# Performance work log

Measured on AMD Instinct MI355X. Metric: run time of the kernel, lower is better.

Reference implementation:

```python
import jax, jax.numpy as jnp
import numpy as np

# ---- fixed configuration (from init_kwargs / sensor='WV3', ratio=4) ----
B, NBANDS, H, W = 4, 8, 512, 512
RATIO = 4
BETA = 0.25
KSIZE = 41                    # MTF kernel size used by gen_mtf
SCALE = 2                     # ceil(ratio / 2), StructuralLoss half-window
MASK_HW = 8                   # half-window used by local_corr_mask
MTF_R = MTF_C = 2             # strided scatter offsets in SpectralLossNocorr
EPS = 1e-20
# WV3 Nyquist gains (one per MS band)
GNYQ = np.asarray([0.325, 0.355, 0.360, 0.350, 0.365, 0.360, 0.335, 0.315])


def gen_mtf_kernel():
    """Per-band Gaussian MTF filter, shape (NBANDS, 1, K, K), sum-normalized."""
    fcut = 1.0 / RATIO
    ax = np.arange(KSIZE) - (KSIZE - 1) / 2.0
    xx, yy = np.meshgrid(ax, ax)
    kerns = []
    for g in GNYQ:
        alpha = np.sqrt(((KSIZE - 1) * (fcut / 2.0)) ** 2 / (-2.0 * np.log(g)))
        k = np.exp(-(xx ** 2 + yy ** 2) / (2.0 * alpha ** 2))
        kerns.append(k / k.sum())
    return np.stack(kerns, axis=0)[:, None].astype(np.float32)


def _boxsum(x, w):
    """Sum over a 2w x 2w sliding window via double cumsum (matches torch ref)."""
    x = jnp.pad(x, ((0, 0), (0, 0), (w, w), (w, w)))
    c = jnp.cumsum(jnp.cumsum(x, axis=-1), axis=-2)
    return (c[..., 2 * w:, 2 * w:] - c[..., :-2 * w, 2 * w:]
            - c[..., 2 * w:, :-2 * w] + c[..., :-2 * w, :-2 * w])


def _xcorr(a, b, w):
    """Local cross-correlation (xcorr_torch). a:(B,Ca,H,W), b:(B,Cb,H,W) broadcast."""
    n = 4.0 * w * w
    da = a - _boxsum(a, w) / n
    db = b - _boxsum(b, w) / n
    s_ab = _boxsum(da * db, w)
    s_aa = _boxsum(da * da, w)
    s_bb = _boxsum(db * db, w)
    return s_ab / (jnp.sqrt(s_aa * s_bb) + EPS)


def _depthconv(x, kern):
    # torch Conv2d(groups=nbands, padding='same') == grouped cross-correlation
    return jax.lax.conv_general_dilated(
        x, kern, (1, 1), 'SAME', feature_group_count=kern.shape[0],
        dimension_numbers=('NCHW', 'OIHW', 'NCHW'))


def _local_corr_mask(inp, kern):
    pan = inp[:, -1:, :, :]          # (B,1,H,W)
    ms = inp[:, :-1, :, :]           # (B,NB,H,W)
    k0 = kern[0:1]                   # first-band MTF kernel (1,1,K,K)
    pad = (KSIZE - 1) // 2
    pan = jnp.pad(pan, ((0, 0), (0, 0), (pad, pad), (pad, pad)), mode='edge')
    pan = jax.lax.conv_general_dilated(
        pan, k0, (1, 1), 'VALID', dimension_numbers=('NCHW', 'OIHW', 'NCHW'))
    return 1.0 - _xcorr(pan, ms, MASK_HW)  # (B,NB,H,W)


def setup_inputs() -> dict:
    key = jax.random.key(0)
    k1, k2, k3 = jax.random.split(key, 3)
    return {
        'outputs': jax.random.normal(k1, (B, NBANDS, H, W), jnp.float32),
        'labels': jax.random.uniform(k2, (B, NBANDS + 1, H, W), jnp.float32),
        'inp': jax.random.uniform(k3, (B, NBANDS + 1, H, W), jnp.float32),
        'mtf_kernel': jnp.asarray(gen_mtf_kernel()),           # frozen param
        'spec_mask': jnp.ones((1, NBANDS, H, W), jnp.float32),  # buffer
    }


def reference(outputs, labels, inp, mtf_kernel, spec_mask):
    # ---- SpectralLossNocorr ----
    x = _depthconv(outputs, mtf_kernel)                      # (B,NB,H,W)
    labels_spec = labels[:, :-1]
    sub = labels_spec[:, :, 2::RATIO, 2::RATIO]              # (B,NB,H/4,W/4)
    y = jnp.zeros_like(x).at[:, :, MTF_R::RATIO, MTF_C::RATIO].set(sub)
    msub = jnp.broadcast_to(spec_mask[:, :, 2::RATIO, 2::RATIO], sub.shape)
    Wm = jnp.zeros_like(x).at[:, :, MTF_R::RATIO, MTF_C::RATIO].set(msub)
    Wm = Wm / jnp.sum(Wm)
    L_spec = jnp.sum(jnp.abs(x * Wm - y * Wm))
    # ---- StructuralLoss (with local_corr_mask threshold) ----
    pan = labels[:, -1:, :, :]
    thr = _local_corr_mask(inp, mtf_kernel)                  # (B,NB,H,W)
    Xc = jnp.maximum(_xcorr(outputs, pan, SCALE), -1.0)      # clamp(min=-1)
    X = 1.0 - Xc
    Y = X * (X > thr)                                        # keep worst pixels
    L_struct = jnp.mean(Y)
    return L_spec + BETA * L_struct
```

## Files before the change

kernel.cpp:

```cpp
#include <hip/hip_runtime.h>
#include <hip/hip_bf16.h>

#define HWSZ   262144
#define IMG    512
#define NBATCH 4
#define NBANDS 8

typedef _Float16 half_t;
typedef _Float16 half2v __attribute__((ext_vector_type(2)));
typedef _Float16 half4v __attribute__((ext_vector_type(4)));
typedef _Float16 half8v __attribute__((ext_vector_type(8)));

__device__ __forceinline__ void blockReduceAtomicAdd(double v, double* target,
                                                     double* red) {
    for (int off = 32; off > 0; off >>= 1) v += __shfl_down(v, off, 64);
    const int wave = threadIdx.x >> 6, lane = threadIdx.x & 63;
    if (lane == 0) red[wave] = v;
    __syncthreads();
    if (threadIdx.x == 0) atomicAdd(target, red[0] + red[1] + red[2] + red[3]);
}

__global__ __launch_bounds__(256) void k_pan_h(const float* __restrict__ inp,
                                               const float* __restrict__ mtf,
                                               float* __restrict__ tmpH) {
    __shared__ float seg[296];
    __shared__ float vrow[41];
    const int tid = threadIdx.x;
    const int b = blockIdx.z, r = blockIdx.y, c0 = blockIdx.x * 256;
    if (tid < 41) vrow[tid] = mtf[20 * 41 + tid] / sqrtf(mtf[20 * 41 + 20]);
    const float* pan = inp + ((long)b * 9 + 8) * HWSZ + (long)r * IMG;
    for (int e = tid; e < 296; e += 256) {
        int c = c0 - 20 + e;
        c = min(max(c, 0), IMG - 1);
        seg[e] = pan[c];
    }
    __syncthreads();
    float s = 0.f;
#pragma unroll
    for (int j = 0; j < 41; ++j) s += vrow[j] * seg[tid + j];
    tmpH[(long)b * HWSZ + (long)r * IMG + c0 + tid] = s;
}

__global__ __launch_bounds__(256) void k_pan_v(const float* __restrict__ tmpH,
                                               const float* __restrict__ mtf,
                                               float* __restrict__ panf) {
    __shared__ float ucol[41];
    const int tid = threadIdx.x;
    const int b = blockIdx.z, r = blockIdx.y, c = blockIdx.x * 256 + tid;
    if (tid < 41) ucol[tid] = mtf[tid * 41 + 20] / sqrtf(mtf[20 * 41 + 20]);
    __syncthreads();
    const float* base = tmpH + (long)b * HWSZ;
    float s = 0.f;
#pragma unroll
    for (int i = 0; i < 41; ++i) {
        int rr = min(max(r - 20 + i, 0), IMG - 1);
        s += ucol[i] * base[(long)rr * IMG + c];
    }
    panf[(long)b * HWSZ + (long)r * IMG + c] = s;
}

template <int W>
__global__ __launch_bounds__(256) void k_da(const float* __restrict__ in,
                                            long inBatchStride,
                                            float* __restrict__ out) {
    constexpr int TS = 32, WIN = 2 * W, NN = 4 * W * W, RE = TS + WIN - 1;
    constexpr int SR = RE;
    constexpr int ST = 33;
    __shared__ float RAW[RE * SR];
    __shared__ float T[RE * ST];
    const int tid = threadIdx.x;
    const int tr0 = blockIdx.y * TS, tc0 = blockIdx.x * TS;
    const float* src = in + (long)blockIdx.z * inBatchStride;
    for (int e = tid; e < RE * RE; e += 256) {
        int r = e / RE, c = e % RE;
        int gr = tr0 - (W - 1) + r, gc = tc0 - (W - 1) + c;
        float v = 0.f;
        if (gr >= 0 && gr < IMG && gc >= 0 && gc < IMG) v = src[(long)gr * IMG + gc];
        RAW[r * SR + c] = v;
    }
    __syncthreads();
    for (int e = tid; e < RE * TS; e += 256) {
        int r = e >> 5, j = e & 31;
        float s = 0.f;
#pragma unroll
        for (int k = 0; k < WIN; ++k) s += RAW[r * SR + j + k];
        T[r * ST + j] = s;
    }
    __syncthreads();
    float* dst = out + (long)blockIdx.z * HWSZ;
    for (int e = tid; e < TS * TS; e += 256) {
        int pr = e >> 5, pc = e & 31;
        float s = 0.f;
#pragma unroll
        for (int k = 0; k < WIN; ++k) s += T[(pr + k) * ST + pc];
        float da = RAW[(pr + W - 1) * SR + (pc + W - 1)] - s * (1.0f / NN);
        dst[(long)(tr0 + pr) * IMG + tc0 + pc] = da;
    }
}

template <int W>
__global__ __launch_bounds__(256) void k_sq(const float* __restrict__ in,
                                            float* __restrict__ out) {
    constexpr int TS = 32, WIN = 2 * W, RE = TS + WIN - 1;
    constexpr int SR = RE, ST = 33;
    __shared__ float RAW[RE * SR];
    __shared__ float T[RE * ST];
    const int tid = threadIdx.x;
    const int tr0 = blockIdx.y * TS, tc0 = blockIdx.x * TS;
    const float* src = in + (long)blockIdx.z * HWSZ;
    for (int e = tid; e < RE * RE; e += 256) {
        int r = e / RE, c = e % RE;
        int gr = tr0 - (W - 1) + r, gc = tc0 - (W - 1) + c;
        float v = 0.f;
        if (gr >= 0 && gr < IMG && gc >= 0 && gc < IMG) v = src[(long)gr * IMG + gc];
        RAW[r * SR + c] = v;
    }
    __syncthreads();
    for (int e = tid; e < RE * TS; e += 256) {
        int r = e >> 5, j = e & 31;
        float s = 0.f;
#pragma unroll
        for (int k = 0; k < WIN; ++k) {
            float v = RAW[r * SR + j + k];
            s += v * v;
        }
        T[r * ST + j] = s;
    }
    __syncthreads();
    float* dst = out + (long)blockIdx.z * HWSZ;
    for (int e = tid; e < TS * TS; e += 256) {
        int pr = e >> 5, pc = e & 31;
        float s = 0.f;
#pragma unroll
        for (int k = 0; k < WIN; ++k) s += T[(pr + k) * ST + pc];
        dst[(long)(tr0 + pr) * IMG + tc0 + pc] = s;
    }
}


template <int W> struct WinDims {
    static constexpr int A  = (W + 3) & ~3;
    static constexpr int NU = A + W + 8;
    static constexpr int NF = (NU + 3) / 4;
    static constexpr int NV = NF * 4;
};

template <int W>
__device__ __forceinline__ void loadRowWin(const float* __restrict__ row, int c0,
                                           float* v) {
    constexpr int A = WinDims<W>::A;
    constexpr int NF = WinDims<W>::NF;
#pragma unroll
    for (int f = 0; f < NF; ++f) {
        const int cb = c0 - A + 4 * f;
        if (cb >= 0 && cb + 3 < IMG) {
            const float4 t = *(const float4*)(row + cb);
            v[4 * f + 0] = t.x; v[4 * f + 1] = t.y;
            v[4 * f + 2] = t.z; v[4 * f + 3] = t.w;
        } else {
#pragma unroll
            for (int u = 0; u < 4; ++u) {
                const int c = cb + u;
                v[4 * f + u] = (c >= 0 && c < IMG) ? row[c] : 0.f;
            }
        }
    }
}

template <int W>
__device__ __forceinline__ void loadRowWinH(const half_t* __restrict__ row, int c0,
                                            float* v) {
    constexpr int A = WinDims<W>::A;
    constexpr int NF = WinDims<W>::NF;
#pragma unroll
    for (int f = 0; f < NF; ++f) {
        const int cb = c0 - A + 4 * f;
        if (cb >= 0 && cb + 3 < IMG) {
            const half4v t = *(const half4v*)(row + cb);
            v[4 * f + 0] = (float)t[0]; v[4 * f + 1] = (float)t[1];
            v[4 * f + 2] = (float)t[2]; v[4 * f + 3] = (float)t[3];
        } else {
#pragma unroll
            for (int u = 0; u < 4; ++u) {
                const int c = cb + u;
                v[4 * f + u] = (c >= 0 && c < IMG) ? (float)row[c] : 0.f;
            }
        }
    }
}

template <int W>
__global__ __launch_bounds__(256) void kHbox(const float* __restrict__ in,
                                             long sB, long sC,
                                             half_t* __restrict__ out) {
    constexpr int A = WinDims<W>::A;
    const int g = blockIdx.x * 256 + threadIdx.x;
    const int c0 = (g & 63) << 3, r = (g >> 6) & 511, z = g >> 15;
    const float* row = in + (long)(z >> 3) * sB + (long)(z & 7) * sC + (long)r * IMG;
    float v[WinDims<W>::NV];
    loadRowWin<W>(row, c0, v);
    float o[8];
    float s = 0.f;
#pragma unroll
    for (int i = A - W + 1; i <= A + W; ++i) s += v[i];
    o[0] = s;
#pragma unroll
    for (int j = 1; j < 8; ++j) {
        s += v[A + W + j] - v[A - W + j];
        o[j] = s;
    }
    half8v h;
#pragma unroll
    for (int j = 0; j < 8; ++j) h[j] = (half_t)o[j];
    *(half8v*)(out + (long)z * HWSZ + (long)r * IMG + c0) = h;
}

template <int W>
__global__ __launch_bounds__(256) void kVda(const half_t* __restrict__ t,
                                            const float* __restrict__ orig,
                                            long sB, long sC,
                                            half_t* __restrict__ out) {
    constexpr int NR = 2 * W + 15, NN = 4 * W * W;
    const int g = blockIdx.x * 256 + threadIdx.x;
    const int cp = (g & 255) * 2;
    const int rc = (g >> 8) & 31, z = g >> 13;
    const int r0 = rc * 16;
    const half_t* tz = t + (long)z * HWSZ + cp;
    float vx[NR], vy[NR];
#pragma unroll
    for (int i = 0; i < NR; ++i) {
        const int rr = r0 - W + 1 + i;
        if (rr >= 0 && rr < IMG) {
            const half2v h = *(const half2v*)(tz + (long)rr * IMG);
            vx[i] = (float)h[0]; vy[i] = (float)h[1];
        } else { vx[i] = 0.f; vy[i] = 0.f; }
    }
    const float* oz = orig + (long)(z >> 3) * sB + (long)(z & 7) * sC + cp;
    half_t* dst = out + (long)z * HWSZ + cp;
    float sx = 0.f, sy = 0.f;
#pragma unroll
    for (int i = 0; i < 2 * W; ++i) { sx += vx[i]; sy += vy[i]; }
#pragma unroll
    for (int j = 0; j < 16; ++j) {
        const float2 o = *(const float2*)(oz + (long)(r0 + j) * IMG);
        half2v h;
        h[0] = (half_t)(o.x - sx * (1.0f / NN));
        h[1] = (half_t)(o.y - sy * (1.0f / NN));
        *(half2v*)(dst + (long)(r0 + j) * IMG) = h;
        if (j < 15) {
            sx += vx[2 * W + j] - vx[j];
            sy += vy[2 * W + j] - vy[j];
        }
    }
}


template <int W>
__device__ __forceinline__ void stageProducts(const half_t* __restrict__ daz,
                                              const float* __restrict__ dsz,
                                              int tr0, int tc0,
                                              unsigned int* L) {
    constexpr int A = WinDims<W>::A;
    constexpr int NU = WinDims<W>::NU;
    constexpr int NV = WinDims<W>::NV;
    constexpr int NRS = 63 + 2 * W;
    constexpr int LP = 65;
    for (int e = threadIdx.x; e < NRS * 8; e += 256) {
        const int i = e >> 3, cg = e & 7;
        const int gr = tr0 - W + 1 + i;
        const int c0 = tc0 + cg * 8;
        unsigned int* dst = L + i * LP + cg * 8;
        if (gr < 0 || gr >= IMG) {
#pragma unroll
            for (int j = 0; j < 8; ++j) dst[j] = 0u;
            continue;
        }
        float va[NV], vs[NV];
        loadRowWinH<W>(daz + (long)gr * IMG, c0, va);
        loadRowWin<W>(dsz + (long)gr * IMG, c0, vs);
        float p1[NV], p2[NV];
#pragma unroll
        for (int k = 0; k < NU; ++k) { p1[k] = va[k] * vs[k]; p2[k] = va[k] * va[k]; }
        float s1 = 0.f, s2 = 0.f;
#pragma unroll
        for (int k = A - W + 1; k <= A + W; ++k) { s1 += p1[k]; s2 += p2[k]; }
#pragma unroll
        for (int j = 0; j < 8; ++j) {
            half2v h;
            h[0] = (half_t)s1; h[1] = (half_t)s2;
            dst[j] = __builtin_bit_cast(unsigned int, h);
            if (j < 7) {
                s1 += p1[A + W + 1 + j] - p1[A - W + 1 + j];
                s2 += p2[A + W + 1 + j] - p2[A - W + 1 + j];
            }
        }
    }
}

__global__ __launch_bounds__(256) void kFusedThr(const half_t* __restrict__ daMS,
                                                 const float* __restrict__ daPAN,
                                                 const float* __restrict__ saa,
                                                 half_t* __restrict__ thr) {
    constexpr int W = 8, LP = 65, NRS = 63 + 2 * W;
    __shared__ unsigned int L[NRS * LP];
    const int z = blockIdx.z, b = z >> 3;
    const int tr0 = blockIdx.y * 64, tc0 = blockIdx.x * 64;
    stageProducts<W>(daMS + (long)z * HWSZ, daPAN + (long)b * HWSZ, tr0, tc0, L);
    __syncthreads();
    const int c = threadIdx.x & 63, q = threadIdx.x >> 6;
    const int ro0 = q * 16;
    float s1 = 0.f, s2 = 0.f;
#pragma unroll
    for (int k = 0; k < 2 * W; ++k) {
        const half2v h = __builtin_bit_cast(half2v, L[(ro0 + k) * LP + c]);
        s1 += (float)h[0]; s2 += (float)h[1];
    }
    const float* sz = saa + (long)b * HWSZ + tc0 + c;
    half_t* tz = thr + (long)z * HWSZ + tc0 + c;
#pragma unroll
    for (int j = 0; j < 16; ++j) {
        const int r = tr0 + ro0 + j;
        const float sa = sz[(long)r * IMG];
        const float den = sqrtf(fmaxf(sa * s2, 0.f)) + 1e-20f;
        tz[(long)r * IMG] = (half_t)(1.0f - s1 / den);
        if (j < 15) {
            const half2v ha = __builtin_bit_cast(half2v, L[(ro0 + j + 2 * W) * LP + c]);
            const half2v hs = __builtin_bit_cast(half2v, L[(ro0 + j) * LP + c]);
            s1 += (float)ha[0] - (float)hs[0];
            s2 += (float)ha[1] - (float)hs[1];
        }
    }
}

__global__ __launch_bounds__(256) void kFusedY(const half_t* __restrict__ daOUT,
                                               const float* __restrict__ dbPAN,
                                               const float* __restrict__ sbb,
                                               const half_t* __restrict__ thr,
                                               double* __restrict__ acc) {
    constexpr int W = 2, LP = 65, NRS = 63 + 2 * W;
    __shared__ unsigned int L[NRS * LP];
    __shared__ double red[4];
    const int z = blockIdx.z, b = z >> 3;
    const int tr0 = blockIdx.y * 64, tc0 = blockIdx.x * 64;
    stageProducts<W>(daOUT + (long)z * HWSZ, dbPAN + (long)b * HWSZ, tr0, tc0, L);
    __syncthreads();
    const int c = threadIdx.x & 63, q = threadIdx.x >> 6;
    const int ro0 = q * 16;
    float s1 = 0.f, s2 = 0.f;
#pragma unroll
    for (int k = 0; k < 2 * W; ++k) {
        const half2v h = __builtin_bit_cast(half2v, L[(ro0 + k) * LP + c]);
        s1 += (float)h[0]; s2 += (float)h[1];
    }
    const float* sz = sbb + (long)b * HWSZ + tc0 + c;
    const half_t* tz = thr + (long)z * HWSZ + tc0 + c;
    double ysum = 0.0;
#pragma unroll
    for (int j = 0; j < 16; ++j) {
        const int r = tr0 + ro0 + j;
        const float sb = sz[(long)r * IMG];
        const float den = sqrtf(fmaxf(s2 * sb, 0.f)) + 1e-20f;
        const float Xc = s1 / den;
        const float X = 1.0f - fmaxf(Xc, -1.0f);
        if (X > (float)tz[(long)r * IMG]) ysum += (double)X;
        if (j < 15) {
            const half2v ha = __builtin_bit_cast(half2v, L[(ro0 + j + 2 * W) * LP + c]);
            const half2v hs = __builtin_bit_cast(half2v, L[(ro0 + j) * LP + c]);
            s1 += (float)ha[0] - (float)hs[0];
            s2 += (float)ha[1] - (float)hs[1];
        }
    }
    blockReduceAtomicAdd(ysum, acc + 2, red);
}

__global__ __launch_bounds__(256) void k_spec_h(const float* __restrict__ outputs,
                                                const float* __restrict__ mtf,
                                                float* __restrict__ tmpS) {
    __shared__ float vrow[41];
    const int g = blockIdx.x * 256 + threadIdx.x;
    const int q = g & 31, r = (g >> 5) & 511, z = g >> 14;
    const int band = z & 7;
    if (threadIdx.x < 41)
        vrow[threadIdx.x] = mtf[band * 1681 + 20 * 41 + threadIdx.x] /
                            sqrtf(mtf[band * 1681 + 20 * 41 + 20]);
    __syncthreads();
    const float* row = outputs + (long)z * HWSZ + (long)r * IMG;
    float v[56];
#pragma unroll
    for (int f = 0; f < 14; ++f) {
        const int cb = 16 * q - 20 + 4 * f;
        if (cb >= 0 && cb + 3 < IMG) {
            const float4 t = *(const float4*)(row + cb);
            v[4 * f + 0] = t.x; v[4 * f + 1] = t.y;
            v[4 * f + 2] = t.z; v[4 * f + 3] = t.w;
        } else {
#pragma unroll
            for (int u = 0; u < 4; ++u) {
                const int cc = cb + u;
                v[4 * f + u] = (cc >= 0 && cc < IMG) ? row[cc] : 0.f;
            }
        }
    }
    float o[4] = {0.f, 0.f, 0.f, 0.f};
#pragma unroll
    for (int j = 0; j < 41; ++j) {
        const float w = vrow[j];
#pragma unroll
        for (int u = 0; u < 4; ++u) o[u] += w * v[2 + 4 * u + j];
    }
    float* dst = tmpS + ((long)z * IMG + r) * 128 + 4 * q;
    *(float4*)dst = make_float4(o[0], o[1], o[2], o[3]);
}

__global__ __launch_bounds__(256) void k_spec_v(const float* __restrict__ tmpS,
                                                const float* __restrict__ labels,
                                                const float* __restrict__ spec,
                                                const float* __restrict__ mtf,
                                                double* __restrict__ acc) {
    __shared__ double redT[4];
    __shared__ double redM[4];
    __shared__ float ucol[41];
    const int g = blockIdx.x * 256 + threadIdx.x;
    const int q = g & 31, rs = (g >> 5) & 127, z = g >> 12;
    const int b = z >> 3, band = z & 7;
    if (threadIdx.x < 41)
        ucol[threadIdx.x] = mtf[band * 1681 + threadIdx.x * 41 + 20] /
                            sqrtf(mtf[band * 1681 + 20 * 41 + 20]);
    __syncthreads();
    const float* base = tmpS + (long)z * IMG * 128 + 4 * q;
    const int rbase = 4 * rs - 18;
    float o[4] = {0.f, 0.f, 0.f, 0.f};
    if (rbase >= 0 && rbase + 40 < IMG) {
#pragma unroll
        for (int i = 0; i < 41; ++i) {
            const float4 v = *(const float4*)(base + (long)(rbase + i) * 128);
            const float w = ucol[i];
            o[0] += w * v.x; o[1] += w * v.y; o[2] += w * v.z; o[3] += w * v.w;
        }
    } else {
        for (int i = 0; i < 41; ++i) {
            const int r = rbase + i;
            if (r >= 0 && r < IMG) {
                const float4 v = *(const float4*)(base + (long)r * 128);
                const float w = ucol[i];
                o[0] += w * v.x; o[1] += w * v.y; o[2] += w * v.z; o[3] += w * v.w;
            }
        }
    }
    const int gr = 2 + 4 * rs;
    float tsum = 0.f, msum = 0.f;
#pragma unroll
    for (int u = 0; u < 4; ++u) {
        const int gc = 2 + 4 * (4 * q + u);
        const float m = spec[(long)band * HWSZ + (long)gr * IMG + gc];
        const float y = labels[((long)b * 9 + band) * HWSZ + (long)gr * IMG + gc];
        tsum += fabsf(o[u] * m - y * m);
        msum += m;
    }
    blockReduceAtomicAdd((double)tsum, acc + 0, redT);
    blockReduceAtomicAdd((double)msum, acc + 1, redM);
}

__global__ void k_final(const double* __restrict__ acc, float* __restrict__ out) {
    double lspec = acc[0] / acc[1];
    double lstruct = acc[2] / (double)(NBATCH * NBANDS * HWSZ);
    out[0] = (float)(lspec + 0.25 * lstruct);
}

extern "C" void kernel_launch(void* const* d_in, const int* in_sizes, int n_in,
                              void* d_out, int out_size, void* d_ws, size_t ws_size,
                              hipStream_t stream) {
    const float* outputs = (const float*)d_in[0];
    const float* labels  = (const float*)d_in[1];
    const float* inp     = (const float*)d_in[2];
    const float* mtf     = (const float*)d_in[3];
    const float* spec    = (const float*)d_in[4];
    float* out = (float*)d_out;

    const long IMGB = (long)HWSZ;
    char* ws = (char*)d_ws;
    double* acc    = (double*)ws;
    float* panf    = (float*)(ws + 1024);
    float* tmpH    = panf   + NBATCH * IMGB;
    float* da_pan8 = tmpH   + NBATCH * IMGB;
    float* saa8    = da_pan8 + NBATCH * IMGB;
    float* db_pan2 = saa8   + NBATCH * IMGB;
    float* sbb2    = db_pan2 + NBATCH * IMGB;
    float* tmpS    = sbb2   + NBATCH * IMGB;
    half_t* hT     = (half_t*)(tmpS + 8 * IMGB);
    half_t* hDA8   = hT   + 32 * IMGB;
    half_t* hDA2   = hDA8 + 32 * IMGB;
    half_t* thrH   = hDA2 + 32 * IMGB;

    hipMemsetAsync(acc, 0, 4 * sizeof(double), stream);

    k_pan_h<<<dim3(2, 512, NBATCH), 256, 0, stream>>>(inp, mtf, tmpH);
    k_pan_v<<<dim3(2, 512, NBATCH), 256, 0, stream>>>(tmpH, mtf, panf);
    k_da<8><<<dim3(16, 16, NBATCH), 256, 0, stream>>>(panf, (long)HWSZ, da_pan8);
    k_sq<8><<<dim3(16, 16, NBATCH), 256, 0, stream>>>(da_pan8, saa8);
    k_da<2><<<dim3(16, 16, NBATCH), 256, 0, stream>>>(labels + 8 * IMGB,
                                                      (long)9 * HWSZ, db_pan2);
    k_sq<2><<<dim3(16, 16, NBATCH), 256, 0, stream>>>(db_pan2, sbb2);

    k_spec_h<<<2048, 256, 0, stream>>>(outputs, mtf, tmpS);
    k_spec_v<<<512, 256, 0, stream>>>(tmpS, labels, spec, mtf, acc);

    kHbox<8><<<4096, 256, 0, stream>>>(inp, 9 * IMGB, IMGB, hT);
    kVda<8><<<1024, 256, 0, stream>>>(hT, inp, 9 * IMGB, IMGB, hDA8);
    kHbox<2><<<4096, 256, 0, stream>>>(outputs, 8 * IMGB, IMGB, hT);
    kVda<2><<<1024, 256, 0, stream>>>(hT, outputs, 8 * IMGB, IMGB, hDA2);

    kFusedThr<<<dim3(8, 8, 32), 256, 0, stream>>>(hDA8, da_pan8, saa8, thrH);
    kFusedY<<<dim3(8, 8, 32), 256, 0, stream>>>(hDA2, db_pan2, sbb2, thrH, acc);

    k_final<<<1, 1, 0, stream>>>(acc, out);
}
```

Before: 312.8 us.

## Fuse box-mean passes into tiled LDS kernel and merge threshold with Y pass

The separate horizontal and vertical box-mean kernels are replaced by one tiled kernel. It stages horizontal window sums in shared memory and computes the vertical sliding sum and mean subtraction in place, so the fp16 intermediate buffer round-trip goes away. The threshold and Y kernels are merged into one: threshold values stay in registers and are never written to and reread from a global half-precision buffer. This cuts launches and global traffic. In exchange, the horizontal sums overlap between tiles and are recomputed, and the merged kernel's longer body may raise register pressure.

```diff
diff --git a/kernel.cpp b/kernel.cpp
--- a/kernel.cpp
+++ b/kernel.cpp
@@ -190,70 +190,57 @@
 }
 
 template <int W>
-__global__ __launch_bounds__(256) void kHbox(const float* __restrict__ in,
-                                             long sB, long sC,
-                                             half_t* __restrict__ out) {
+__global__ __launch_bounds__(256) void kDAtile(const float* __restrict__ in,
+                                               long sB, long sC,
+                                               half_t* __restrict__ out) {
     constexpr int A = WinDims<W>::A;
-    const int g = blockIdx.x * 256 + threadIdx.x;
-    const int c0 = (g & 63) << 3, r = (g >> 6) & 511, z = g >> 15;
-    const float* row = in + (long)(z >> 3) * sB + (long)(z & 7) * sC + (long)r * IMG;
-    float v[WinDims<W>::NV];
-    loadRowWin<W>(row, c0, v);
-    float o[8];
+    constexpr int NV = WinDims<W>::NV;
+    constexpr int NRS = 63 + 2 * W;
+    constexpr int LP = 65;
+    constexpr int NN = 4 * W * W;
+    __shared__ float T[NRS * LP];
+    const int z = blockIdx.z;
+    const int tr0 = blockIdx.y * 64, tc0 = blockIdx.x * 64;
+    const float* img = in + (long)(z >> 3) * sB + (long)(z & 7) * sC;
+
+    for (int e = threadIdx.x; e < NRS * 8; e += 256) {
+        const int i = e >> 3, cg = e & 7;
+        const int gr = tr0 - W + 1 + i;
+        float* dst = &T[i * LP + cg * 8];
+        if (gr < 0 || gr >= IMG) {
+#pragma unroll
+            for (int j = 0; j < 8; ++j) dst[j] = 0.f;
+            continue;
+        }
+        float v[NV];
+        loadRowWin<W>(img + (long)gr * IMG, tc0 + cg * 8, v);
+        float s = 0.f;
+#pragma unroll
+        for (int k = A - W + 1; k <= A + W; ++k) s += v[k];
+        dst[0] = s;
+#pragma unroll
+        for (int j = 1; j < 8; ++j) {
+            s += v[A + W + j] - v[A - W + j];
+            dst[j] = s;
+        }
+    }
+    __syncthreads();
+
+    const int c = threadIdx.x & 63, q = threadIdx.x >> 6;
+    const int ro0 = q * 16;
     float s = 0.f;
 #pragma unroll
-    for (int i = A - W + 1; i <= A + W; ++i) s += v[i];
-    o[0] = s;
-#pragma unroll
-    for (int j = 1; j < 8; ++j) {
-        s += v[A + W + j] - v[A - W + j];
-        o[j] = s;
-    }
-    half8v h;
-#pragma unroll
-    for (int j = 0; j < 8; ++j) h[j] = (half_t)o[j];
-    *(half8v*)(out + (long)z * HWSZ + (long)r * IMG + c0) = h;
-}
-
-template <int W>
-__global__ __launch_bounds__(256) void kVda(const half_t* __restrict__ t,
-                                            const float* __restrict__ orig,
-                                            long sB, long sC,
-                                            half_t* __restrict__ out) {
-    constexpr int NR = 2 * W + 15, NN = 4 * W * W;
-    const int g = blockIdx.x * 256 + threadIdx.x;
-    const int cp = (g & 255) * 2;
-    const int rc = (g >> 8) & 31, z = g >> 13;
-    const int r0 = rc * 16;
-    const half_t* tz = t + (long)z * HWSZ + cp;
-    float vx[NR], vy[NR];
-#pragma unroll
-    for (int i = 0; i < NR; ++i) {
-        const int rr = r0 - W + 1 + i;
-        if (rr >= 0 && rr < IMG) {
-            const half2v h = *(const half2v*)(tz + (long)rr * IMG);
-            vx[i] = (float)h[0]; vy[i] = (float)h[1];
-        } else { vx[i] = 0.f; vy[i] = 0.f; }
-    }
-    const float* oz = orig + (long)(z >> 3) * sB + (long)(z & 7) * sC + cp;
-    half_t* dst = out + (long)z * HWSZ + cp;
-    float sx = 0.f, sy = 0.f;
-#pragma unroll
-    for (int i = 0; i < 2 * W; ++i) { sx += vx[i]; sy += vy[i]; }
+    for (int k = 0; k < 2 * W; ++k) s += T[(ro0 + k) * LP + c];
+    const float* oz = img + tc0 + c;
+    half_t* dz = out + (long)z * HWSZ + tc0 + c;
 #pragma unroll
     for (int j = 0; j < 16; ++j) {
-        const float2 o = *(const float2*)(oz + (long)(r0 + j) * IMG);
-        half2v h;
-        h[0] = (half_t)(o.x - sx * (1.0f / NN));
-        h[1] = (half_t)(o.y - sy * (1.0f / NN));
-        *(half2v*)(dst + (long)(r0 + j) * IMG) = h;
-        if (j < 15) {
-            sx += vx[2 * W + j] - vx[j];
-            sy += vy[2 * W + j] - vy[j];
-        }
-    }
-}
-
+        const int r = tr0 + ro0 + j;
+        const float o = oz[(long)r * IMG];
+        dz[(long)r * IMG] = (half_t)(o - s * (1.0f / NN));
+        if (j < 15) s += T[(ro0 + j + 2 * W) * LP + c] - T[(ro0 + j) * LP + c];
+    }
+}
 
 template <int W>
 __device__ __forceinline__ void stageProducts(const half_t* __restrict__ daz,
@@ -297,77 +284,76 @@
     }
 }
 
-__global__ __launch_bounds__(256) void kFusedThr(const half_t* __restrict__ daMS,
-                                                 const float* __restrict__ daPAN,
-                                                 const float* __restrict__ saa,
-                                                 half_t* __restrict__ thr) {
-    constexpr int W = 8, LP = 65, NRS = 63 + 2 * W;
-    __shared__ unsigned int L[NRS * LP];
-    const int z = blockIdx.z, b = z >> 3;
-    const int tr0 = blockIdx.y * 64, tc0 = blockIdx.x * 64;
-    stageProducts<W>(daMS + (long)z * HWSZ, daPAN + (long)b * HWSZ, tr0, tc0, L);
-    __syncthreads();
-    const int c = threadIdx.x & 63, q = threadIdx.x >> 6;
-    const int ro0 = q * 16;
-    float s1 = 0.f, s2 = 0.f;
-#pragma unroll
-    for (int k = 0; k < 2 * W; ++k) {
-        const half2v h = __builtin_bit_cast(half2v, L[(ro0 + k) * LP + c]);
-        s1 += (float)h[0]; s2 += (float)h[1];
-    }
-    const float* sz = saa + (long)b * HWSZ + tc0 + c;
-    half_t* tz = thr + (long)z * HWSZ + tc0 + c;
-#pragma unroll
-    for (int j = 0; j < 16; ++j) {
-        const int r = tr0 + ro0 + j;
-        const float sa = sz[(long)r * IMG];
-        const float den = sqrtf(fmaxf(sa * s2, 0.f)) + 1e-20f;
-        tz[(long)r * IMG] = (half_t)(1.0f - s1 / den);
-        if (j < 15) {
-            const half2v ha = __builtin_bit_cast(half2v, L[(ro0 + j + 2 * W) * LP + c]);
-            const half2v hs = __builtin_bit_cast(half2v, L[(ro0 + j) * LP + c]);
-            s1 += (float)ha[0] - (float)hs[0];
-            s2 += (float)ha[1] - (float)hs[1];
-        }
-    }
-}
-
-__global__ __launch_bounds__(256) void kFusedY(const half_t* __restrict__ daOUT,
-                                               const float* __restrict__ dbPAN,
-                                               const float* __restrict__ sbb,
-                                               const half_t* __restrict__ thr,
-                                               double* __restrict__ acc) {
-    constexpr int W = 2, LP = 65, NRS = 63 + 2 * W;
-    __shared__ unsigned int L[NRS * LP];
+__global__ __launch_bounds__(256) void kFusedXY(const half_t* __restrict__ daMS,
+                                                const float* __restrict__ daPAN,
+                                                const float* __restrict__ saa,
+                                                const half_t* __restrict__ daOUT,
+                                                const float* __restrict__ dbPAN,
+                                                const float* __restrict__ sbb,
+                                                double* __restrict__ acc) {
+    constexpr int LP = 65;
+    constexpr int NRS8 = 63 + 16;
+    __shared__ unsigned int L[NRS8 * LP];
     __shared__ double red[4];
     const int z = blockIdx.z, b = z >> 3;
     const int tr0 = blockIdx.y * 64, tc0 = blockIdx.x * 64;
-    stageProducts<W>(daOUT + (long)z * HWSZ, dbPAN + (long)b * HWSZ, tr0, tc0, L);
-    __syncthreads();
     const int c = threadIdx.x & 63, q = threadIdx.x >> 6;
     const int ro0 = q * 16;
-    float s1 = 0.f, s2 = 0.f;
-#pragma unroll
-    for (int k = 0; k < 2 * W; ++k) {
-        const half2v h = __builtin_bit_cast(half2v, L[(ro0 + k) * LP + c]);
-        s1 += (float)h[0]; s2 += (float)h[1];
-    }
-    const float* sz = sbb + (long)b * HWSZ + tc0 + c;
-    const half_t* tz = thr + (long)z * HWSZ + tc0 + c;
+
+    float thrv[16];
+    {
+        constexpr int W = 8;
+        stageProducts<W>(daMS + (long)z * HWSZ, daPAN + (long)b * HWSZ,
+                         tr0, tc0, L);
+        __syncthreads();
+        float s1 = 0.f, s2 = 0.f;
+#pragma unroll
+        for (int k = 0; k < 2 * W; ++k) {
+            const half2v h = __builtin_bit_cast(half2v, L[(ro0 + k) * LP + c]);
+            s1 += (float)h[0]; s2 += (float)h[1];
+        }
+        const float* sz = saa + (long)b * HWSZ + tc0 + c;
+#pragma unroll
+        for (int j = 0; j < 16; ++j) {
+            const int r = tr0 + ro0 + j;
+            const float sa = sz[(long)r * IMG];
+            const float den = sqrtf(fmaxf(sa * s2, 0.f)) + 1e-20f;
+            thrv[j] = 1.0f - s1 / den;
+            if (j < 15) {
+                const half2v ha = __builtin_bit_cast(half2v, L[(ro0 + j + 2 * W) * LP + c]);
+                const half2v hs = __builtin_bit_cast(half2v, L[(ro0 + j) * LP + c]);
+                s1 += (float)ha[0] - (float)hs[0];
+                s2 += (float)ha[1] - (float)hs[1];
+            }
+        }
+        __syncthreads();
+    }
     double ysum = 0.0;
-#pragma unroll
-    for (int j = 0; j < 16; ++j) {
-        const int r = tr0 + ro0 + j;
-        const float sb = sz[(long)r * IMG];
-        const float den = sqrtf(fmaxf(s2 * sb, 0.f)) + 1e-20f;
-        const float Xc = s1 / den;
-        const float X = 1.0f - fmaxf(Xc, -1.0f);
-        if (X > (float)tz[(long)r * IMG]) ysum += (double)X;
-        if (j < 15) {
-            const half2v ha = __builtin_bit_cast(half2v, L[(ro0 + j + 2 * W) * LP + c]);
-            const half2v hs = __builtin_bit_cast(half2v, L[(ro0 + j) * LP + c]);
-            s1 += (float)ha[0] - (float)hs[0];
-            s2 += (float)ha[1] - (float)hs[1];
+    {
+        constexpr int W = 2;
+        stageProducts<W>(daOUT + (long)z * HWSZ, dbPAN + (long)b * HWSZ,
+                         tr0, tc0, L);
+        __syncthreads();
+        float s1 = 0.f, s2 = 0.f;
+#pragma unroll
+        for (int k = 0; k < 2 * W; ++k) {
+            const half2v h = __builtin_bit_cast(half2v, L[(ro0 + k) * LP + c]);
+            s1 += (float)h[0]; s2 += (float)h[1];
+        }
+        const float* sz = sbb + (long)b * HWSZ + tc0 + c;
+#pragma unroll
+        for (int j = 0; j < 16; ++j) {
+            const float sb = sz[(long)(tr0 + ro0 + j) * IMG];
+            const float den = sqrtf(fmaxf(s2 * sb, 0.f)) + 1e-20f;
+            const float Xc = s1 / den;
+            const float X = 1.0f - fmaxf(Xc, -1.0f);
+            if (X > thrv[j]) ysum += (double)X;
+            if (j < 15) {
+                const half2v ha = __builtin_bit_cast(half2v, L[(ro0 + j + 2 * W) * LP + c]);
+                const half2v hs = __builtin_bit_cast(half2v, L[(ro0 + j) * LP + c]);
+                s1 += (float)ha[0] - (float)hs[0];
+                s2 += (float)ha[1] - (float)hs[1];
+            }
         }
     }
     blockReduceAtomicAdd(ysum, acc + 2, red);
@@ -487,10 +473,8 @@
     float* db_pan2 = saa8   + NBATCH * IMGB;
     float* sbb2    = db_pan2 + NBATCH * IMGB;
     float* tmpS    = sbb2   + NBATCH * IMGB;
-    half_t* hT     = (half_t*)(tmpS + 8 * IMGB);
-    half_t* hDA8   = hT   + 32 * IMGB;
+    half_t* hDA8   = (half_t*)(tmpS + 8 * IMGB);
     half_t* hDA2   = hDA8 + 32 * IMGB;
-    half_t* thrH   = hDA2 + 32 * IMGB;
 
     hipMemsetAsync(acc, 0, 4 * sizeof(double), stream);
 
@@ -505,13 +489,11 @@
     k_spec_h<<<2048, 256, 0, stream>>>(outputs, mtf, tmpS);
     k_spec_v<<<512, 256, 0, stream>>>(tmpS, labels, spec, mtf, acc);
 
-    kHbox<8><<<4096, 256, 0, stream>>>(inp, 9 * IMGB, IMGB, hT);
-    kVda<8><<<1024, 256, 0, stream>>>(hT, inp, 9 * IMGB, IMGB, hDA8);
-    kHbox<2><<<4096, 256, 0, stream>>>(outputs, 8 * IMGB, IMGB, hT);
-    kVda<2><<<1024, 256, 0, stream>>>(hT, outputs, 8 * IMGB, IMGB, hDA2);
-
-    kFusedThr<<<dim3(8, 8, 32), 256, 0, stream>>>(hDA8, da_pan8, saa8, thrH);
-    kFusedY<<<dim3(8, 8, 32), 256, 0, stream>>>(hDA2, db_pan2, sbb2, thrH, acc);
+    kDAtile<8><<<dim3(8, 8, 32), 256, 0, stream>>>(inp, 9 * IMGB, IMGB, hDA8);
+    kDAtile<2><<<dim3(8, 8, 32), 256, 0, stream>>>(outputs, 8 * IMGB, IMGB, hDA2);
+
+    kFusedXY<<<dim3(8, 8, 32), 256, 0, stream>>>(hDA8, da_pan8, saa8,
+                                                 hDA2, db_pan2, sbb2, acc);
 
     k_final<<<1, 1, 0, stream>>>(acc, out);
 }
```

Result: faster. 304.1 us (-2.8%).
